# Kernel optimization log

Hardware: AMD Instinct MI355X
Metric: run time of the kernel (lower is better)

The kernel has to match this reference:

```python
import jax, jax.numpy as jnp
import numpy as np

B, D, L = 2, 1024, 4096   # batch, channels (= num_heads), seq len
FS = 4                    # filter_size
DEPTH = 11                # ceil(log2((L-1)/(FS-1)+1))
LN_EPS = 1e-5


def setup_inputs() -> dict:
    key = jax.random.key(0)
    ks = jax.random.split(key, 7)
    return {
        "x": jax.random.normal(ks[0], (B, D, L), jnp.float32),
        "h0": jax.random.normal(ks[1], (D, 1, FS), jnp.float32) * 0.2,
        "h1": jax.random.normal(ks[2], (D, 1, FS), jnp.float32) * 0.2,
        "w_mix": jax.random.normal(ks[3], (D, D), jnp.float32) / np.sqrt(D),
        "b_mix": jnp.zeros((D,), jnp.float32),
        "ln_gamma": jnp.ones((D,), jnp.float32),
        "ln_beta": jnp.zeros((D,), jnp.float32),
    }


def _dw_conv(a, h, dilation):
    # depthwise (groups = D) dilated conv1d, cross-correlation like torch
    return jax.lax.conv_general_dilated(
        a, h, window_strides=(1,), padding='VALID',
        rhs_dilation=(dilation,),
        dimension_numbers=('NCH', 'OIH', 'NCH'),
        feature_group_count=D)


def reference(x, h0, h1, w_mix, b_mix, ln_gamma, ln_beta):
    # --- multires conv tree ---
    a = x
    dilation = 1
    a_list, b_list = [], []
    for _ in range(DEPTH):
        pad = dilation * (FS - 1)
        ap = jnp.pad(a, ((0, 0), (0, 0), (pad, 0)))  # left causal pad
        b = _dw_conv(ap, h1, dilation)
        a = _dw_conv(ap, h0, dilation)
        a_list.append(a)
        b_list.append(b)
        dilation *= 2
    # --- gated combination across scales (deepest level first) ---
    a_rev = a_list[::-1]
    b_rev = b_list[::-1]
    y = jnp.zeros_like(x)
    gated = None
    for i in range(DEPTH):
        if i + 1 < DEPTH:
            gated = jax.nn.sigmoid(a_rev[i]) * b_rev[i + 1]
        # last iteration reuses the previous gated tensor (matches original)
        y = y + gated
    # --- 1x1 channel mix (Dropout1d is identity in eval) + residual ---
    mixed = jnp.einsum('oc,bcl->bol', w_mix, y) + b_mix[None, :, None]
    z = mixed + x
    # --- LayerNorm over channel dim ---
    mu = jnp.mean(z, axis=1, keepdims=True)
    var = jnp.mean(jnp.square(z - mu), axis=1, keepdims=True)
    out = (z - mu) * jax.lax.rsqrt(var + LN_EPS)
    out = out * ln_gamma[None, :, None] + ln_beta[None, :, None]
    return out
```

## Files before the change

### kernel.cpp

```cpp
#include <hip/hip_runtime.h>
#include <hip/hip_bf16.h>

#define NB 2
#define ND 1024
#define NL 4096
#define NFS 4
#define NDEPTH 11
#define LN_EPS 1e-5f

#define BM 128
#define BN 128
#define BK 32
#define NKI (ND / BK)

#define CPAD 384
#define CBUF (CPAD + NL)

typedef __bf16 bf16x8 __attribute__((ext_vector_type(8)));
typedef float f32x4 __attribute__((ext_vector_type(4)));

__device__ __forceinline__ unsigned short f2bf(float f) {
    __hip_bfloat16 h = __float2bfloat16(f);
    unsigned short u;
    __builtin_memcpy(&u, &h, 2);
    return u;
}

__device__ __forceinline__ float bf2f(unsigned short u) {
    unsigned int ui = (unsigned int)u << 16;
    float f;
    __builtin_memcpy(&f, &ui, 4);
    return f;
}

__device__ __forceinline__ unsigned int pack2bf(float lo, float hi) {
    return (unsigned int)f2bf(lo) | ((unsigned int)f2bf(hi) << 16);
}

__device__ __forceinline__ float sigm(float v) {
    return __builtin_amdgcn_rcpf(1.f + __expf(-v));
}

__device__ __forceinline__ void llds16(const void* g, void* l) {
    __builtin_amdgcn_global_load_lds(
        (const __attribute__((address_space(1))) unsigned int*)g,
        (__attribute__((address_space(3))) unsigned int*)l, 16, 0, 0);
}

__global__ __launch_bounds__(256) void wconv_kernel(const float* __restrict__ w,
                                                    unsigned short* __restrict__ wbf) {
    const int idx8 = (blockIdx.x * 256 + threadIdx.x) * 8;
    const float4 v0 = *reinterpret_cast<const float4*>(w + idx8);
    const float4 v1 = *reinterpret_cast<const float4*>(w + idx8 + 4);
    uint4 o;
    o.x = pack2bf(v0.x, v0.y);
    o.y = pack2bf(v0.z, v0.w);
    o.z = pack2bf(v1.x, v1.y);
    o.w = pack2bf(v1.z, v1.w);
    *reinterpret_cast<uint4*>(wbf + idx8) = o;
}

__global__ __launch_bounds__(256) void conv_cascade_kernel(const float* __restrict__ x,
                                                           const float* __restrict__ h0,
                                                           const float* __restrict__ h1,
                                                           unsigned short* __restrict__ ybf) {
    __shared__ float a_sh[2 * CBUF];
    const int row = blockIdx.x;
    const int d = row & (ND - 1);
    const int t = threadIdx.x;

#pragma unroll
    for (int j = 0; j < 2; ++j) {
        a_sh[j * CBUF + t] = 0.f;
        if (t < CPAD - 256) a_sh[j * CBUF + 256 + t] = 0.f;
    }

    const float* xrow = x + (size_t)row * NL;

    float h0c[NFS], h1c[NFS];
#pragma unroll
    for (int k = 0; k < NFS; ++k) {
        h0c[k] = h0[d * NFS + k];
        h1c[k] = h1[d * NFS + k];
    }

    float cur[16], yacc[16], bprev[16];
#pragma unroll
    for (int i = 0; i < 16; ++i) {
        cur[i] = xrow[i * 256 + t];
        a_sh[CPAD + i * 256 + t] = cur[i];
        yacc[i] = 0.f;
        bprev[i] = 0.f;
    }
    __syncthreads();

    int rb = 0, wb = CBUF;
    int dil = 1;
#pragma unroll 1
    for (int lev = 0; lev < 7; ++lev) {
        const int off1 = rb + CPAD + t - dil;
        const int off2 = rb + CPAD + t - 2 * dil;
        const int off3 = rb + CPAD + t - 3 * dil;
        float anew[16], bnew[16];
#pragma unroll
        for (int i = 0; i < 16; ++i) {
            const float a0 = cur[i];
            const float a1 = a_sh[off1 + i * 256];
            const float a2 = a_sh[off2 + i * 256];
            const float a3 = a_sh[off3 + i * 256];
            anew[i] = h0c[3] * a0 + h0c[2] * a1 + h0c[1] * a2 + h0c[0] * a3;
            bnew[i] = h1c[3] * a0 + h1c[2] * a1 + h1c[1] * a2 + h1c[0] * a3;
        }
#pragma unroll
        for (int i = 0; i < 16; ++i) a_sh[wb + CPAD + i * 256 + t] = anew[i];

        if (lev >= 1) {
            const float sc = (lev == 1) ? 2.f : 1.f;
#pragma unroll
            for (int i = 0; i < 16; ++i)
                yacc[i] += sc * sigm(anew[i]) * bprev[i];
        }
#pragma unroll
        for (int i = 0; i < 16; ++i) {
            cur[i] = anew[i];
            bprev[i] = bnew[i];
        }
        dil <<= 1;
        const int tmp = rb; rb = wb; wb = tmp;
        __syncthreads();
    }

    {
        const int off1 = rb + CPAD + t - 128;
        const int off2 = rb + CPAD + t - 256;
        const int off3 = rb + CPAD + t - 384;
        float anew[16], bnew[16];
#pragma unroll
        for (int i = 0; i < 16; ++i) {
            const float a0 = cur[i];
            const float a1 = a_sh[off1 + i * 256];
            const float a2 = a_sh[off2 + i * 256];
            const float a3 = a_sh[off3 + i * 256];
            anew[i] = h0c[3] * a0 + h0c[2] * a1 + h0c[1] * a2 + h0c[0] * a3;
            bnew[i] = h1c[3] * a0 + h1c[2] * a1 + h1c[1] * a2 + h1c[0] * a3;
        }
#pragma unroll
        for (int i = 0; i < 16; ++i) {
            yacc[i] += sigm(anew[i]) * bprev[i];
            cur[i] = anew[i];
            bprev[i] = bnew[i];
        }
    }

    {
        float anew[16], bnew[16];
#pragma unroll
        for (int i = 0; i < 16; ++i) {
            const float a0 = cur[i];
            const float a1 = (i >= 1) ? cur[i - 1] : 0.f;
            const float a2 = (i >= 2) ? cur[i - 2] : 0.f;
            const float a3 = (i >= 3) ? cur[i - 3] : 0.f;
            anew[i] = h0c[3] * a0 + h0c[2] * a1 + h0c[1] * a2 + h0c[0] * a3;
            bnew[i] = h1c[3] * a0 + h1c[2] * a1 + h1c[1] * a2 + h1c[0] * a3;
        }
#pragma unroll
        for (int i = 0; i < 16; ++i) {
            yacc[i] += sigm(anew[i]) * bprev[i];
            cur[i] = anew[i];
            bprev[i] = bnew[i];
        }
    }

    {
        float anew[16], bnew[16];
#pragma unroll
        for (int i = 0; i < 16; ++i) {
            const float a0 = cur[i];
            const float a1 = (i >= 2) ? cur[i - 2] : 0.f;
            const float a2 = (i >= 4) ? cur[i - 4] : 0.f;
            const float a3 = (i >= 6) ? cur[i - 6] : 0.f;
            anew[i] = h0c[3] * a0 + h0c[2] * a1 + h0c[1] * a2 + h0c[0] * a3;
            bnew[i] = h1c[3] * a0 + h1c[2] * a1 + h1c[1] * a2 + h1c[0] * a3;
        }
#pragma unroll
        for (int i = 0; i < 16; ++i) {
            yacc[i] += sigm(anew[i]) * bprev[i];
            cur[i] = anew[i];
            bprev[i] = bnew[i];
        }
    }

#pragma unroll
    for (int i = 0; i < 16; ++i) {
        const float a0 = cur[i];
        const float a1 = (i >= 4) ? cur[i - 4] : 0.f;
        const float a2 = (i >= 8) ? cur[i - 8] : 0.f;
        const float a3 = (i >= 12) ? cur[i - 12] : 0.f;
        const float an = h0c[3] * a0 + h0c[2] * a1 + h0c[1] * a2 + h0c[0] * a3;
        yacc[i] += sigm(an) * bprev[i];
    }

#pragma unroll
    for (int i = 0; i < 16; ++i)
        ybf[(size_t)row * NL + i * 256 + t] = f2bf(yacc[i]);
}

__global__ __launch_bounds__(256) void transpose_kernel(const unsigned short* __restrict__ ybf,
                                                        unsigned short* __restrict__ yT) {
    __shared__ unsigned short tile[64][66];
    const int l0 = blockIdx.x * 64;
    const int c0 = blockIdx.y * 64;
    const int b = blockIdx.z;
    const int t = threadIdx.x;
    const int li = t & 63, cg = t >> 6;
#pragma unroll
    for (int k = 0; k < 16; ++k) {
        const int ci = cg * 16 + k;
        tile[ci][li] = ybf[(size_t)(b * ND + c0 + ci) * NL + l0 + li];
    }
    __syncthreads();
    const int ci2 = t & 63, lg = t >> 6;
#pragma unroll
    for (int k = 0; k < 16; ++k) {
        const int li2 = lg * 16 + k;
        yT[((size_t)b * NL + l0 + li2) * ND + c0 + ci2] = tile[ci2][li2];
    }
}

__global__ __launch_bounds__(256) void gemm_kernel(const unsigned short* __restrict__ wbf,
                                                   const unsigned short* __restrict__ yT,
                                                   const float* __restrict__ bmix,
                                                   unsigned short* __restrict__ mixed) {
    __shared__ unsigned short As[2][BM][BK];
    __shared__ unsigned short Bs[2][BN][BK];

    const int n0 = blockIdx.x * BN;
    const int m0 = blockIdx.y * BM;
    const int b = blockIdx.z;
    const int t = threadIdx.x;
    const int lane = t & 63, wid = t >> 6;
    const int wr = wid >> 1, wc = wid & 1;
    const int fr = lane & 15;
    const int fk = (lane >> 4) * 8;

    const int srow = wid * 32 + (lane >> 2);
    const int sk = (lane & 3) * 8;
    const unsigned short* Ag = wbf + (size_t)(m0 + srow) * ND + sk;
    const unsigned short* Bg = yT + ((size_t)b * NL + n0 + srow) * ND + sk;
    unsigned short* AsD0[2] = {&As[0][wid * 32][0], &As[1][wid * 32][0]};
    unsigned short* AsD1[2] = {&As[0][wid * 32 + 16][0], &As[1][wid * 32 + 16][0]};
    unsigned short* BsD0[2] = {&Bs[0][wid * 32][0], &Bs[1][wid * 32][0]};
    unsigned short* BsD1[2] = {&Bs[0][wid * 32 + 16][0], &Bs[1][wid * 32 + 16][0]};

    f32x4 acc[4][4];
#pragma unroll
    for (int mi = 0; mi < 4; ++mi)
#pragma unroll
        for (int ni = 0; ni < 4; ++ni)
            acc[mi][ni] = (f32x4){0.f, 0.f, 0.f, 0.f};

    llds16(Ag, AsD0[0]);
    llds16(Ag + 16 * ND, AsD1[0]);
    llds16(Bg, BsD0[0]);
    llds16(Bg + 16 * ND, BsD1[0]);
    asm volatile("s_waitcnt vmcnt(0)" ::: "memory");
    __builtin_amdgcn_s_barrier();

    int cur = 0;
#pragma unroll 1
    for (int ki = 0; ki < NKI; ++ki) {
        if (ki + 1 < NKI) {
            const int kt = (ki + 1) * BK;
            llds16(Ag + kt, AsD0[cur ^ 1]);
            llds16(Ag + kt + 16 * ND, AsD1[cur ^ 1]);
            llds16(Bg + kt, BsD0[cur ^ 1]);
            llds16(Bg + kt + 16 * ND, BsD1[cur ^ 1]);
        }

        bf16x8 af[4], bv[4];
#pragma unroll
        for (int mi = 0; mi < 4; ++mi)
            af[mi] = *reinterpret_cast<const bf16x8*>(&As[cur][wr * 64 + mi * 16 + fr][fk]);
#pragma unroll
        for (int ni = 0; ni < 4; ++ni)
            bv[ni] = *reinterpret_cast<const bf16x8*>(&Bs[cur][wc * 64 + ni * 16 + fr][fk]);
#pragma unroll
        for (int mi = 0; mi < 4; ++mi)
#pragma unroll
            for (int ni = 0; ni < 4; ++ni)
                acc[mi][ni] = __builtin_amdgcn_mfma_f32_16x16x32_bf16(af[mi], bv[ni],
                                                                      acc[mi][ni], 0, 0, 0);

        asm volatile("s_waitcnt vmcnt(0)" ::: "memory");
        __builtin_amdgcn_s_barrier();
        cur ^= 1;
    }

    const size_t bbase = (size_t)b * ND * NL;
#pragma unroll
    for (int mi = 0; mi < 4; ++mi) {
#pragma unroll
        for (int r = 0; r < 4; ++r) {
            const int o = m0 + wr * 64 + mi * 16 + (lane >> 4) * 4 + r;
            const float bm = bmix[o];
            const size_t rowbase = bbase + (size_t)o * NL;
#pragma unroll
            for (int ni = 0; ni < 4; ++ni) {
                const int l = n0 + wc * 64 + ni * 16 + fr;
                mixed[rowbase + l] = f2bf(acc[mi][ni][r] + bm);
            }
        }
    }
}

__global__ __launch_bounds__(512) void ln_kernel(const unsigned short* __restrict__ mixed,
                                                 const float* __restrict__ x,
                                                 const float* __restrict__ gamma,
                                                 const float* __restrict__ beta,
                                                 float* __restrict__ out) {
    const int b = blockIdx.y;
    const int l0 = blockIdx.x * 32;
    const int tl = threadIdx.x & 31, tg = threadIdx.x >> 5;
    const size_t base = (size_t)b * ND * NL + l0 + tl;

    float zv[64];
    float s = 0.f, q = 0.f;
#pragma unroll
    for (int j = 0; j < 64; ++j) {
        const size_t idx = base + (size_t)(tg + j * 16) * NL;
        const float v = bf2f(mixed[idx]) + x[idx];
        zv[j] = v;
        s += v;
        q += v * v;
    }

    __shared__ float sred[16][33], qred[16][33];
    __shared__ float mu_s[32], rs_s[32];
    sred[tg][tl] = s;
    qred[tg][tl] = q;
    __syncthreads();
    if (tg == 0) {
        float S = 0.f, Q = 0.f;
#pragma unroll
        for (int g = 0; g < 16; ++g) {
            S += sred[g][tl];
            Q += qred[g][tl];
        }
        const float mu = S * (1.f / ND);
        const float var = Q * (1.f / ND) - mu * mu;
        mu_s[tl] = mu;
        rs_s[tl] = rsqrtf(var + LN_EPS);
    }
    __syncthreads();
    const float mu = mu_s[tl], rs = rs_s[tl];
#pragma unroll
    for (int j = 0; j < 64; ++j) {
        const int c = tg + j * 16;
        out[base + (size_t)c * NL] = (zv[j] - mu) * rs * gamma[c] + beta[c];
    }
}

extern "C" void kernel_launch(void* const* d_in, const int* in_sizes, int n_in,
                              void* d_out, int out_size, void* d_ws, size_t ws_size,
                              hipStream_t stream) {
    (void)in_sizes; (void)n_in; (void)out_size; (void)ws_size;
    const float* x = (const float*)d_in[0];
    const float* h0 = (const float*)d_in[1];
    const float* h1 = (const float*)d_in[2];
    const float* wmix = (const float*)d_in[3];
    const float* bmix = (const float*)d_in[4];
    const float* gamma = (const float*)d_in[5];
    const float* beta = (const float*)d_in[6];
    float* out = (float*)d_out;

    char* ws = (char*)d_ws;
    unsigned short* ybf = (unsigned short*)(ws);
    unsigned short* yT = (unsigned short*)(ws + (size_t)16 * 1024 * 1024);
    unsigned short* wbf = (unsigned short*)(ws + (size_t)32 * 1024 * 1024);
    unsigned short* mixed = (unsigned short*)(ws + (size_t)34 * 1024 * 1024);

    wconv_kernel<<<dim3(ND * ND / (256 * 8)), 256, 0, stream>>>(wmix, wbf);
    conv_cascade_kernel<<<dim3(NB * ND), 256, 0, stream>>>(x, h0, h1, ybf);
    transpose_kernel<<<dim3(NL / 64, ND / 64, NB), 256, 0, stream>>>(ybf, yT);
    gemm_kernel<<<dim3(NL / BN, ND / BM, NB), 256, 0, stream>>>(wbf, yT, bmix, mixed);
    ln_kernel<<<dim3(NL / 32, NB), 512, 0, stream>>>(mixed, x, gamma, beta, out);
}
```

Baseline: 108.7 us.

## Remap conv cascade to contiguous 4-element chunks with vectorized LDS and global access

The conv cascade kernel now has each thread own four contiguous groups of 4 sequence elements (float4) instead of 16 elements strided by 256. Global loads, shared-memory reads and writes, and the bf16 output store become 128-bit vector accesses. The first two dilation levels reuse in-register neighbours, and the register-only tail needs fewer levels. The causal pad grows to 1536, so more LDS is used per block, which may lower occupancy.

```diff
diff --git a/kernel.cpp b/kernel.cpp
--- a/kernel.cpp
+++ b/kernel.cpp
@@ -13,7 +13,7 @@
 #define BK 32
 #define NKI (ND / BK)
 
-#define CPAD 384
+#define CPAD 1536
 #define CBUF (CPAD + NL)
 
 typedef __bf16 bf16x8 __attribute__((ext_vector_type(8)));
@@ -70,10 +70,10 @@
     const int t = threadIdx.x;
 
 #pragma unroll
-    for (int j = 0; j < 2; ++j) {
-        a_sh[j * CBUF + t] = 0.f;
-        if (t < CPAD - 256) a_sh[j * CBUF + 256 + t] = 0.f;
-    }
+    for (int j = 0; j < 2; ++j)
+#pragma unroll
+        for (int i = 0; i < CPAD / 256; ++i)
+            a_sh[j * CBUF + i * 256 + t] = 0.f;
 
     const float* xrow = x + (size_t)row * NL;
 
@@ -84,125 +84,120 @@
         h1c[k] = h1[d * NFS + k];
     }
 
-    float cur[16], yacc[16], bprev[16];
-#pragma unroll
-    for (int i = 0; i < 16; ++i) {
-        cur[i] = xrow[i * 256 + t];
-        a_sh[CPAD + i * 256 + t] = cur[i];
-        yacc[i] = 0.f;
-        bprev[i] = 0.f;
+    float cur[4][4], yacc[4][4], bprev[4][4];
+#pragma unroll
+    for (int c = 0; c < 4; ++c) {
+        const float4 v = *reinterpret_cast<const float4*>(xrow + c * 1024 + t * 4);
+        cur[c][0] = v.x; cur[c][1] = v.y; cur[c][2] = v.z; cur[c][3] = v.w;
+        *reinterpret_cast<float4*>(&a_sh[CPAD + c * 1024 + t * 4]) = v;
+#pragma unroll
+        for (int j = 0; j < 4; ++j) { yacc[c][j] = 0.f; bprev[c][j] = 0.f; }
     }
     __syncthreads();
 
     int rb = 0, wb = CBUF;
-    int dil = 1;
+
+#define CONV_CHUNK(c, A1, A2, A3, SC, WB)                                            \
+    {                                                                                \
+        float an[4], bn[4];                                                          \
+        _Pragma("unroll") for (int j = 0; j < 4; ++j) {                              \
+            an[j] = h0c[3] * cur[c][j] + h0c[2] * (A1)[j] + h0c[1] * (A2)[j] +       \
+                    h0c[0] * (A3)[j];                                                \
+            bn[j] = h1c[3] * cur[c][j] + h1c[2] * (A1)[j] + h1c[1] * (A2)[j] +       \
+                    h1c[0] * (A3)[j];                                                \
+        }                                                                            \
+        if (WB) {                                                                    \
+            float4 wv; wv.x = an[0]; wv.y = an[1]; wv.z = an[2]; wv.w = an[3];       \
+            *reinterpret_cast<float4*>(&a_sh[wb + CPAD + (c)*1024 + t * 4]) = wv;    \
+        }                                                                            \
+        if ((SC) > 0.f) {                                                            \
+            _Pragma("unroll") for (int j = 0; j < 4; ++j)                            \
+                yacc[c][j] += (SC)*sigm(an[j]) * bprev[c][j];                        \
+        }                                                                            \
+        _Pragma("unroll") for (int j = 0; j < 4; ++j) {                              \
+            cur[c][j] = an[j];                                                       \
+            bprev[c][j] = bn[j];                                                     \
+        }                                                                            \
+    }
+
+#pragma unroll
+    for (int c = 0; c < 4; ++c) {
+        const int A = rb + CPAD + c * 1024 + t * 4;
+        const float4 m1 = *reinterpret_cast<const float4*>(&a_sh[A - 4]);
+        const float a1[4] = {m1.w, cur[c][0], cur[c][1], cur[c][2]};
+        const float a2[4] = {m1.z, m1.w, cur[c][0], cur[c][1]};
+        const float a3[4] = {m1.y, m1.z, m1.w, cur[c][0]};
+        CONV_CHUNK(c, a1, a2, a3, 0.f, 1)
+    }
+    { const int tmp = rb; rb = wb; wb = tmp; }
+    __syncthreads();
+
+#pragma unroll
+    for (int c = 0; c < 4; ++c) {
+        const int A = rb + CPAD + c * 1024 + t * 4;
+        const float4 m1 = *reinterpret_cast<const float4*>(&a_sh[A - 4]);
+        const float4 m2 = *reinterpret_cast<const float4*>(&a_sh[A - 8]);
+        const float a1[4] = {m1.z, m1.w, cur[c][0], cur[c][1]};
+        const float a2[4] = {m1.x, m1.y, m1.z, m1.w};
+        const float a3[4] = {m2.z, m2.w, m1.x, m1.y};
+        CONV_CHUNK(c, a1, a2, a3, 2.f, 1)
+    }
+    { const int tmp = rb; rb = wb; wb = tmp; }
+    __syncthreads();
+
+    int dil = 4;
 #pragma unroll 1
-    for (int lev = 0; lev < 7; ++lev) {
-        const int off1 = rb + CPAD + t - dil;
-        const int off2 = rb + CPAD + t - 2 * dil;
-        const int off3 = rb + CPAD + t - 3 * dil;
-        float anew[16], bnew[16];
-#pragma unroll
-        for (int i = 0; i < 16; ++i) {
-            const float a0 = cur[i];
-            const float a1 = a_sh[off1 + i * 256];
-            const float a2 = a_sh[off2 + i * 256];
-            const float a3 = a_sh[off3 + i * 256];
-            anew[i] = h0c[3] * a0 + h0c[2] * a1 + h0c[1] * a2 + h0c[0] * a3;
-            bnew[i] = h1c[3] * a0 + h1c[2] * a1 + h1c[1] * a2 + h1c[0] * a3;
-        }
-#pragma unroll
-        for (int i = 0; i < 16; ++i) a_sh[wb + CPAD + i * 256 + t] = anew[i];
-
-        if (lev >= 1) {
-            const float sc = (lev == 1) ? 2.f : 1.f;
-#pragma unroll
-            for (int i = 0; i < 16; ++i)
-                yacc[i] += sc * sigm(anew[i]) * bprev[i];
-        }
-#pragma unroll
-        for (int i = 0; i < 16; ++i) {
-            cur[i] = anew[i];
-            bprev[i] = bnew[i];
-        }
+    for (int lev = 2; lev <= 8; ++lev) {
+#pragma unroll
+        for (int c = 0; c < 4; ++c) {
+            const int A = rb + CPAD + c * 1024 + t * 4;
+            const float4 b1 = *reinterpret_cast<const float4*>(&a_sh[A - dil]);
+            const float4 b2 = *reinterpret_cast<const float4*>(&a_sh[A - 2 * dil]);
+            const float4 b3 = *reinterpret_cast<const float4*>(&a_sh[A - 3 * dil]);
+            const float a1[4] = {b1.x, b1.y, b1.z, b1.w};
+            const float a2[4] = {b2.x, b2.y, b2.z, b2.w};
+            const float a3[4] = {b3.x, b3.y, b3.z, b3.w};
+            CONV_CHUNK(c, a1, a2, a3, 1.f, 1)
+        }
+        { const int tmp = rb; rb = wb; wb = tmp; }
         dil <<= 1;
-        const int tmp = rb; rb = wb; wb = tmp;
         __syncthreads();
     }
 
-    {
-        const int off1 = rb + CPAD + t - 128;
-        const int off2 = rb + CPAD + t - 256;
-        const int off3 = rb + CPAD + t - 384;
-        float anew[16], bnew[16];
-#pragma unroll
-        for (int i = 0; i < 16; ++i) {
-            const float a0 = cur[i];
-            const float a1 = a_sh[off1 + i * 256];
-            const float a2 = a_sh[off2 + i * 256];
-            const float a3 = a_sh[off3 + i * 256];
-            anew[i] = h0c[3] * a0 + h0c[2] * a1 + h0c[1] * a2 + h0c[0] * a3;
-            bnew[i] = h1c[3] * a0 + h1c[2] * a1 + h1c[1] * a2 + h1c[0] * a3;
-        }
-#pragma unroll
-        for (int i = 0; i < 16; ++i) {
-            yacc[i] += sigm(anew[i]) * bprev[i];
-            cur[i] = anew[i];
-            bprev[i] = bnew[i];
-        }
-    }
-
-    {
-        float anew[16], bnew[16];
-#pragma unroll
-        for (int i = 0; i < 16; ++i) {
-            const float a0 = cur[i];
-            const float a1 = (i >= 1) ? cur[i - 1] : 0.f;
-            const float a2 = (i >= 2) ? cur[i - 2] : 0.f;
-            const float a3 = (i >= 3) ? cur[i - 3] : 0.f;
-            anew[i] = h0c[3] * a0 + h0c[2] * a1 + h0c[1] * a2 + h0c[0] * a3;
-            bnew[i] = h1c[3] * a0 + h1c[2] * a1 + h1c[1] * a2 + h1c[0] * a3;
-        }
-#pragma unroll
-        for (int i = 0; i < 16; ++i) {
-            yacc[i] += sigm(anew[i]) * bprev[i];
-            cur[i] = anew[i];
-            bprev[i] = bnew[i];
-        }
-    }
-
-    {
-        float anew[16], bnew[16];
-#pragma unroll
-        for (int i = 0; i < 16; ++i) {
-            const float a0 = cur[i];
-            const float a1 = (i >= 2) ? cur[i - 2] : 0.f;
-            const float a2 = (i >= 4) ? cur[i - 4] : 0.f;
-            const float a3 = (i >= 6) ? cur[i - 6] : 0.f;
-            anew[i] = h0c[3] * a0 + h0c[2] * a1 + h0c[1] * a2 + h0c[0] * a3;
-            bnew[i] = h1c[3] * a0 + h1c[2] * a1 + h1c[1] * a2 + h1c[0] * a3;
-        }
-#pragma unroll
-        for (int i = 0; i < 16; ++i) {
-            yacc[i] += sigm(anew[i]) * bprev[i];
-            cur[i] = anew[i];
-            bprev[i] = bnew[i];
-        }
-    }
-
-#pragma unroll
-    for (int i = 0; i < 16; ++i) {
-        const float a0 = cur[i];
-        const float a1 = (i >= 4) ? cur[i - 4] : 0.f;
-        const float a2 = (i >= 8) ? cur[i - 8] : 0.f;
-        const float a3 = (i >= 12) ? cur[i - 12] : 0.f;
-        const float an = h0c[3] * a0 + h0c[2] * a1 + h0c[1] * a2 + h0c[0] * a3;
-        yacc[i] += sigm(an) * bprev[i];
-    }
-
-#pragma unroll
-    for (int i = 0; i < 16; ++i)
-        ybf[(size_t)row * NL + i * 256 + t] = f2bf(yacc[i]);
+#pragma unroll
+    for (int c = 0; c < 4; ++c) {
+        const int A = rb + CPAD + c * 1024 + t * 4;
+        const float4 b1 = *reinterpret_cast<const float4*>(&a_sh[A - 512]);
+        const float4 b2 = *reinterpret_cast<const float4*>(&a_sh[A - 1024]);
+        const float4 b3 = *reinterpret_cast<const float4*>(&a_sh[A - 1536]);
+        const float a1[4] = {b1.x, b1.y, b1.z, b1.w};
+        const float a2[4] = {b2.x, b2.y, b2.z, b2.w};
+        const float a3[4] = {b3.x, b3.y, b3.z, b3.w};
+        CONV_CHUNK(c, a1, a2, a3, 1.f, 0)
+    }
+
+#pragma unroll
+    for (int c = 0; c < 4; ++c) {
+#pragma unroll
+        for (int j = 0; j < 4; ++j) {
+            const float a1 = (c >= 1) ? cur[c - 1][j] : 0.f;
+            const float a2 = (c >= 2) ? cur[c - 2][j] : 0.f;
+            const float a3 = (c >= 3) ? cur[c - 3][j] : 0.f;
+            const float an = h0c[3] * cur[c][j] + h0c[2] * a1 + h0c[1] * a2 + h0c[0] * a3;
+            yacc[c][j] += sigm(an) * bprev[c][j];
+        }
+    }
+#undef CONV_CHUNK
+
+#pragma unroll
+    for (int c = 0; c < 4; ++c) {
+        ushort4 o;
+        o.x = f2bf(yacc[c][0]);
+        o.y = f2bf(yacc[c][1]);
+        o.z = f2bf(yacc[c][2]);
+        o.w = f2bf(yacc[c][3]);
+        *reinterpret_cast<ushort4*>(ybf + (size_t)row * NL + c * 1024 + t * 4) = o;
+    }
 }
 
 __global__ __launch_bounds__(256) void transpose_kernel(const unsigned short* __restrict__ ybf,
```

Result: faster. 105.8 us (-2.7%).
